# Optimization experiments

Hardware: AMD Instinct MI355X
Metric: run time of the kernel (lower is better)

The kernel has to match this reference:

```python
import jax, jax.numpy as jnp
import numpy as np

B, T, L, D, H = 8, 8192, 256, 512, 8
HD = D // H  # head_dim = 64


def setup_inputs() -> dict:
    key = jax.random.key(0)
    ks = jax.random.split(key, 6)
    s = 0.02
    return {
        "x": jax.random.normal(ks[0], (B, T, D), jnp.float32),
        "query": jax.random.normal(ks[1], (B, L, D), jnp.float32),
        "Wq": jax.random.normal(ks[2], (D, D), jnp.float32) * s,
        "bq": jnp.zeros((D,), jnp.float32),
        "Wkv": jax.random.normal(ks[3], (D, 2 * D), jnp.float32) * s,
        "bkv": jnp.zeros((2 * D,), jnp.float32),
        "Wproj": jax.random.normal(ks[4], (D, D), jnp.float32) * s,
        "bproj": jnp.zeros((D,), jnp.float32),
    }


def reference(x, query, Wq, bq, Wkv, bkv, Wproj, bproj):
    scale = HD ** (-0.5)
    # projections (weights stored [in, out]; equivalent to torch Linear with W.T)
    q = (query @ Wq + bq).reshape(B, L, H, HD).transpose(0, 2, 1, 3)   # [B,H,L,hd]
    kv = (x @ Wkv + bkv).reshape(B, T, 2, H, HD)
    k = kv[:, :, 0].transpose(0, 2, 1, 3)                              # [B,H,T,hd]
    v = kv[:, :, 1].transpose(0, 2, 1, 3)                              # [B,H,T,hd]
    # scaled dot-product attention, full L x T scores as in original
    attn = jnp.einsum("bhld,bhtd->bhlt", q * scale, k)                 # [B,H,L,T]
    attn = jax.nn.softmax(attn, axis=-1)
    out = jnp.einsum("bhlt,bhtd->bhld", attn, v)                       # [B,H,L,hd]
    out = out.transpose(0, 2, 1, 3).reshape(B, L, D)
    return out @ Wproj + bproj
```

## Files before the change

kernel.cpp:

```cpp
#include <hip/hip_runtime.h>
#include <hip/hip_bf16.h>
#include <cstdint>
#include <cstddef>

typedef __bf16 bf16_t;
typedef __bf16 bf16x8 __attribute__((ext_vector_type(8)));
typedef __bf16 bf16x4 __attribute__((ext_vector_type(4)));
typedef float  f32x4  __attribute__((ext_vector_type(4)));

#define DEVI __device__ __forceinline__

constexpr int B_ = 8, T_ = 8192, L_ = 256, D_ = 512, H_ = 8, HD_ = 64;
constexpr float SCALE_LOG2E = 0.125f * 1.44269504088896340736f;
constexpr int NSPLIT = 8;

DEVI float fast_exp2(float x) {
#if __has_builtin(__builtin_amdgcn_exp2f)
  return __builtin_amdgcn_exp2f(x);
#else
  return exp2f(x);
#endif
}

DEVI void async16(void* lds_base, const void* gptr, int lane) {
#if __has_builtin(__builtin_amdgcn_global_load_lds)
  __builtin_amdgcn_global_load_lds(
      (__attribute__((address_space(1))) void*)gptr,
      (__attribute__((address_space(3))) void*)lds_base, 16, 0, 0);
  (void)lane;
#else
  ((bf16x8*)lds_base)[lane] = *(const bf16x8*)gptr;
#endif
}

__global__ __launch_bounds__(256) void cvt_f32_to_bf16(
    const float* __restrict__ in, bf16_t* __restrict__ out, int n4) {
  int stride = gridDim.x * blockDim.x;
  for (int i = blockIdx.x * blockDim.x + threadIdx.x; i < n4; i += stride) {
    float4 v = ((const float4*)in)[i];
    bf16x4 o;
    o[0] = (bf16_t)v.x; o[1] = (bf16_t)v.y; o[2] = (bf16_t)v.z; o[3] = (bf16_t)v.w;
    ((bf16x4*)out)[i] = o;
  }
}

__global__ __launch_bounds__(256) void transpose_cvt(
    const float* __restrict__ W, bf16_t* __restrict__ WT, int K, int N, float scale) {
  __shared__ float tile[32][33];
  const int tx = threadIdx.x & 31, ty = threadIdx.x >> 5;
  const int n0 = blockIdx.x * 32, k0 = blockIdx.y * 32;
#pragma unroll
  for (int i = 0; i < 4; ++i)
    tile[ty + i * 8][tx] = W[(size_t)(k0 + ty + i * 8) * N + n0 + tx];
  __syncthreads();
#pragma unroll
  for (int i = 0; i < 4; ++i)
    WT[(size_t)(n0 + ty + i * 8) * K + k0 + tx] = (bf16_t)(tile[tx][ty + i * 8] * scale);
}

template <int MODE>
__global__ __launch_bounds__(256, 4) void gemm_bf16(
    const bf16_t* __restrict__ A, const bf16_t* __restrict__ BT,
    const float* __restrict__ bias, float bscale,
    bf16_t* __restrict__ out0,
    float* __restrict__ outf) {
  constexpr int K = 512;
  __shared__ __align__(16) union SM {
    bf16_t stage[2][128 * 64];
    bf16_t cs[128 * 136];
  } sm;

  const int tid = threadIdx.x;
  const int w = tid >> 6, lane = tid & 63;
  const int m0 = blockIdx.x * 128, n0 = blockIdx.y * 128;
  const int wm = w & 1, wn = w >> 1;

  f32x4 acc[4][4] = {};

  const int sw = ((lane & 7) ^ ((lane >> 3) & 7)) * 8;
  const bf16_t* aG = A + (size_t)(m0 + w * 32 + (lane >> 3)) * K + sw;
  const bf16_t* bG = BT + (size_t)(n0 + w * 32 + (lane >> 3)) * K + sw;
  bf16_t* aL = &sm.stage[0][(w * 32) * 64];
  bf16_t* bL = &sm.stage[1][(w * 32) * 64];

  for (int k0 = 0; k0 < K; k0 += 64) {
#pragma unroll
    for (int i = 0; i < 4; ++i) {
      async16(aL + i * (8 * 64), aG + k0 + (size_t)(i * 8) * K, lane);
      async16(bL + i * (8 * 64), bG + k0 + (size_t)(i * 8) * K, lane);
    }
    __syncthreads();
#pragma unroll
    for (int kk = 0; kk < 2; ++kk) {
      bf16x8 af[4], bfr[4];
      const int cc = ((kk * 4 + (lane >> 4)) ^ (lane & 7)) * 8;
#pragma unroll
      for (int mt = 0; mt < 4; ++mt)
        af[mt] = *(const bf16x8*)&sm.stage[0][(wm * 64 + mt * 16 + (lane & 15)) * 64 + cc];
#pragma unroll
      for (int nt = 0; nt < 4; ++nt)
        bfr[nt] = *(const bf16x8*)&sm.stage[1][(wn * 64 + nt * 16 + (lane & 15)) * 64 + cc];
#pragma unroll
      for (int mt = 0; mt < 4; ++mt)
#pragma unroll
        for (int nt = 0; nt < 4; ++nt)
          acc[mt][nt] = __builtin_amdgcn_mfma_f32_16x16x32_bf16(af[mt], bfr[nt], acc[mt][nt], 0, 0, 0);
    }
    __syncthreads();
  }

  if (MODE == 2) {
#pragma unroll
    for (int nt = 0; nt < 4; ++nt) {
      const int col = n0 + wn * 64 + nt * 16 + (lane & 15);
      const float bv = bias[col];
#pragma unroll
      for (int mt = 0; mt < 4; ++mt)
#pragma unroll
        for (int r = 0; r < 4; ++r) {
          const int row = m0 + wm * 64 + mt * 16 + (lane >> 4) * 4 + r;
          outf[(size_t)row * D_ + col] = acc[mt][nt][r] + bv;
        }
    }
    return;
  }

#pragma unroll
  for (int nt = 0; nt < 4; ++nt) {
    const int col = wn * 64 + nt * 16 + (lane & 15);
    const float bv = bias[n0 + col] * bscale;
#pragma unroll
    for (int mt = 0; mt < 4; ++mt)
#pragma unroll
      for (int r = 0; r < 4; ++r) {
        const int row = wm * 64 + mt * 16 + (lane >> 4) * 4 + r;
        sm.cs[row * 136 + col] = (bf16_t)(acc[mt][nt][r] + bv);
      }
  }
  __syncthreads();

#pragma unroll
  for (int i = 0; i < 8; ++i) {
    const int c = tid + i * 256;
    const int row = c >> 4, col = (c & 15) * 8;
    const int gr = m0 + row;
    const int b = gr >> 8, l = gr & 255;
    const int h = (n0 + col) >> 6, hd = (n0 + col) & 63;
    *(float4*)&out0[((size_t)(b * 8 + h) * L_ + l) * 64 + hd] =
        *(const float4*)&sm.cs[row * 136 + col];
  }
}

__global__ __launch_bounds__(512, 2) void gemm_kv(
    const bf16_t* __restrict__ A, const bf16_t* __restrict__ BT,
    const float* __restrict__ bias,
    bf16_t* __restrict__ kh, bf16_t* __restrict__ vTh) {
  constexpr int K = 512;
  __shared__ __align__(16) union SM {
    bf16_t stage[2][2][256 * 64];
    bf16_t cs[128 * 264];
  } sm;

  const int tid = threadIdx.x;
  const int w = tid >> 6, lane = tid & 63;
  const int wm = w & 1, wn = w >> 1;

  const int b = blockIdx.x;
  const int xcd = b & 7, idx = b >> 3;
  const int m0 = ((xcd << 5) | (idx >> 2)) * 256;
  const int n0 = (idx & 3) * 256;

  f32x4 acc[8][4] = {};

  const int sw = ((lane & 7) ^ ((lane >> 3) & 7)) * 8;
  const int rl = w * 8 + (lane >> 3);

  {
    bf16_t* As = sm.stage[0][0];
    bf16_t* Bs = sm.stage[0][1];
#pragma unroll
    for (int i = 0; i < 4; ++i)
      async16(As + (i * 64 + w * 8) * 64, A + (size_t)(m0 + i * 64 + rl) * K + sw, lane);
#pragma unroll
    for (int i = 0; i < 4; ++i)
      async16(Bs + (i * 64 + w * 8) * 64, BT + (size_t)(n0 + i * 64 + rl) * K + sw, lane);
  }

  for (int t = 0; t < 8; ++t) {
    __syncthreads();
    if (t < 7) {
      bf16_t* As = sm.stage[(t + 1) & 1][0];
      bf16_t* Bs = sm.stage[(t + 1) & 1][1];
      const int k0 = (t + 1) * 64;
#pragma unroll
      for (int i = 0; i < 4; ++i)
        async16(As + (i * 64 + w * 8) * 64, A + (size_t)(m0 + i * 64 + rl) * K + k0 + sw, lane);
#pragma unroll
      for (int i = 0; i < 4; ++i)
        async16(Bs + (i * 64 + w * 8) * 64, BT + (size_t)(n0 + i * 64 + rl) * K + k0 + sw, lane);
    }
    const bf16_t* As = sm.stage[t & 1][0];
    const bf16_t* Bs = sm.stage[t & 1][1];
#pragma unroll
    for (int kk = 0; kk < 2; ++kk) {
      const int cc = ((kk * 4 + (lane >> 4)) ^ (lane & 7)) * 8;
      bf16x8 bfr[4];
#pragma unroll
      for (int nt = 0; nt < 4; ++nt)
        bfr[nt] = *(const bf16x8*)&Bs[(wn * 64 + nt * 16 + (lane & 15)) * 64 + cc];
#pragma unroll
      for (int mh = 0; mh < 2; ++mh) {
        bf16x8 af[4];
#pragma unroll
        for (int mt = 0; mt < 4; ++mt)
          af[mt] = *(const bf16x8*)&As[(wm * 128 + (mh * 4 + mt) * 16 + (lane & 15)) * 64 + cc];
#pragma unroll
        for (int mt = 0; mt < 4; ++mt)
#pragma unroll
          for (int nt = 0; nt < 4; ++nt)
            acc[mh * 4 + mt][nt] = __builtin_amdgcn_mfma_f32_16x16x32_bf16(
                af[mt], bfr[nt], acc[mh * 4 + mt][nt], 0, 0, 0);
      }
    }
  }
  __syncthreads();

  float bv[4];
#pragma unroll
  for (int nt = 0; nt < 4; ++nt)
    bv[nt] = bias[n0 + wn * 64 + nt * 16 + (lane & 15)];

  if (n0 < 512) {
#pragma unroll
    for (int mh = 0; mh < 2; ++mh) {
      if (wm == mh) {
#pragma unroll
        for (int a = 0; a < 8; ++a)
#pragma unroll
          for (int nt = 0; nt < 4; ++nt)
#pragma unroll
            for (int r = 0; r < 4; ++r) {
              const int rowL = a * 16 + (lane >> 4) * 4 + r;
              const int col = wn * 64 + nt * 16 + (lane & 15);
              sm.cs[rowL * 264 + col] = (bf16_t)(acc[a][nt][r] + bv[nt]);
            }
      }
      __syncthreads();
#pragma unroll
      for (int i = 0; i < 8; ++i) {
        const int c = tid + i * 512;
        const int row = c >> 5, col = (c & 31) * 8;
        const int gr = m0 + mh * 128 + row;
        const int bb = gr >> 13, tt = gr & 8191;
        const int h = (n0 + col) >> 6, hd = (n0 + col) & 63;
        *(float4*)&kh[((size_t)(bb * 8 + h) * T_ + tt) * 64 + hd] =
            *(const float4*)&sm.cs[row * 264 + col];
      }
      __syncthreads();
    }
  } else {
    const int bb = m0 >> 13, t0 = m0 & 8191;
#pragma unroll
    for (int nh = 0; nh < 2; ++nh) {
      if ((wn >> 1) == nh) {
#pragma unroll
        for (int a = 0; a < 8; ++a)
#pragma unroll
          for (int nt = 0; nt < 4; ++nt)
#pragma unroll
            for (int r = 0; r < 4; ++r) {
              const int row = wm * 128 + a * 16 + (lane >> 4) * 4 + r;
              const int colL = (wn & 1) * 64 + nt * 16 + (lane & 15);
              sm.cs[colL * 264 + row] = (bf16_t)(acc[a][nt][r] + bv[nt]);
            }
      }
      __syncthreads();
#pragma unroll
      for (int i = 0; i < 8; ++i) {
        const int c = tid + i * 512;
        const int colL = c >> 5, tb = (c & 31) * 8;
        const int ch = (n0 - 512) + nh * 128 + colL;
        const int h = ch >> 6, hd = ch & 63;
        *(float4*)&vTh[((size_t)(bb * 8 + h) * 64 + hd) * T_ + t0 + tb] =
            *(const float4*)&sm.cs[colL * 264 + tb];
      }
      __syncthreads();
    }
  }
}

__global__ __launch_bounds__(256, 4) void attn_fwd(
    const bf16_t* __restrict__ qg, const bf16_t* __restrict__ kg,
    const bf16_t* __restrict__ vg, float* __restrict__ Opart,
    float* __restrict__ lbuf) {
  __shared__ __align__(16) bf16_t KPs[10240];
  __shared__ __align__(16) bf16_t Vs[4 * 64 * 32];
  bf16_t* Ks = KPs;
  bf16_t* Ps = KPs;
  bf16_t* Qs = KPs;

  const int n = blockIdx.x;
  const int split = n & 7, qt = (n >> 3) & 3, bh = n >> 5;
  const int tid = threadIdx.x;
  const int w = tid >> 6, lane = tid & 63;

  {
    const bf16_t* src = qg + ((size_t)bh * L_ + qt * 64) * 64;
    const int row = w * 16 + (lane >> 2);
#pragma unroll
    for (int hh = 0; hh < 2; ++hh)
      async16(&Qs[hh * 2048 + (w * 16) * 32],
              src + (size_t)row * 64 + hh * 32 + (lane & 3) * 8, lane);
  }
  __syncthreads();

  bf16x8 aq[2];
#pragma unroll
  for (int hh = 0; hh < 2; ++hh)
    aq[hh] = *(const bf16x8*)&Qs[hh * 2048 + (w * 16 + (lane & 15)) * 32 + (lane >> 4) * 8];
  __syncthreads();

  bf16x8 ones;
#pragma unroll
  for (int j = 0; j < 8; ++j) ones[j] = (bf16_t)1.0f;

  f32x4 O[4] = {};
  f32x4 lacc = {0.f, 0.f, 0.f, 0.f};

  const int kt0 = split * (T_ / 128 / NSPLIT);
  for (int kt = kt0; kt < kt0 + T_ / 128 / NSPLIT; ++kt) {
#pragma unroll
    for (int hh = 0; hh < 2; ++hh)
#pragma unroll
      for (int i = 0; i < 2; ++i) {
        const int trow = kt * 128 + w * 32 + i * 16 + (lane >> 2);
        async16(&Ks[hh * 4096 + (w * 32 + i * 16) * 32],
                kg + ((size_t)bh * T_ + trow) * 64 + hh * 32 + (lane & 3) * 8, lane);
      }
#pragma unroll
    for (int kc = 0; kc < 4; ++kc) {
      const int hd = w * 16 + (lane >> 2);
      async16(&Vs[kc * 2048 + (w * 16) * 32],
              vg + ((size_t)bh * 64 + hd) * T_ + kt * 128 + kc * 32 + (lane & 3) * 8, lane);
    }
    __syncthreads();

    f32x4 S[8];
#pragma unroll
    for (int nt = 0; nt < 8; ++nt) {
      bf16x8 b0 = *(const bf16x8*)&Ks[0 * 4096 + (nt * 16 + (lane & 15)) * 32 + (lane >> 4) * 8];
      bf16x8 b1 = *(const bf16x8*)&Ks[1 * 4096 + (nt * 16 + (lane & 15)) * 32 + (lane >> 4) * 8];
      f32x4 s = {0.f, 0.f, 0.f, 0.f};
      s = __builtin_amdgcn_mfma_f32_16x16x32_bf16(aq[0], b0, s, 0, 0, 0);
      s = __builtin_amdgcn_mfma_f32_16x16x32_bf16(aq[1], b1, s, 0, 0, 0);
#pragma unroll
      for (int r = 0; r < 4; ++r) s[r] = fast_exp2(s[r]);
      S[nt] = s;
    }

    __syncthreads();

#pragma unroll
    for (int nt = 0; nt < 8; ++nt)
#pragma unroll
      for (int r = 0; r < 4; ++r) {
        const int rp = w * 16 + (lane >> 4) * 4 + r;
        Ps[(nt >> 1) * 2560 + rp * 40 + (nt & 1) * 16 + (lane & 15)] = (bf16_t)S[nt][r];
      }

    __syncthreads();

#pragma unroll
    for (int kc = 0; kc < 4; ++kc) {
      bf16x8 ap = *(const bf16x8*)&Ps[kc * 2560 + (w * 16 + (lane & 15)) * 40 + (lane >> 4) * 8];
      lacc = __builtin_amdgcn_mfma_f32_16x16x32_bf16(ap, ones, lacc, 0, 0, 0);
#pragma unroll
      for (int n2 = 0; n2 < 4; ++n2) {
        bf16x8 bv = *(const bf16x8*)&Vs[kc * 2048 + (n2 * 16 + (lane & 15)) * 32 + (lane >> 4) * 8];
        O[n2] = __builtin_amdgcn_mfma_f32_16x16x32_bf16(ap, bv, O[n2], 0, 0, 0);
      }
    }
    __syncthreads();
  }

  const int part = ((bh * 4 + qt) * NSPLIT + split);
  float* op = Opart + (size_t)part * 64 * 64;
#pragma unroll
  for (int n2 = 0; n2 < 4; ++n2) {
#pragma unroll
    for (int r = 0; r < 4; ++r) {
      const int row = w * 16 + (lane >> 4) * 4 + r;
      op[(size_t)row * 64 + n2 * 16 + (lane & 15)] = O[n2][r];
    }
  }
  if ((lane & 15) == 0) {
    float* lb = lbuf + (size_t)part * 64;
#pragma unroll
    for (int r = 0; r < 4; ++r)
      lb[w * 16 + (lane >> 4) * 4 + r] = lacc[r];
  }
}

__global__ __launch_bounds__(256) void attn_combine(
    const float* __restrict__ Opart, const float* __restrict__ lbuf,
    bf16_t* __restrict__ og) {
  const int blk = blockIdx.x;
  const int bh = blk >> 2, qt = blk & 3;
  const int tid = threadIdx.x;
  const int row = tid >> 2, c0 = (tid & 3) * 16;
  float L = 0.f;
#pragma unroll
  for (int s = 0; s < NSPLIT; ++s) L += lbuf[((size_t)blk * NSPLIT + s) * 64 + row];
  const float inv = 1.f / L;
  f32x4 acc[4] = {};
  const float* ob = Opart + (size_t)blk * NSPLIT * 4096 + row * 64 + c0;
#pragma unroll
  for (int s = 0; s < NSPLIT; ++s)
#pragma unroll
    for (int j = 0; j < 4; ++j) {
      f32x4 v = *(const f32x4*)&ob[s * 4096 + j * 4];
      acc[j] += v;
    }
  const int b = bh >> 3, h = bh & 7;
  bf16_t* dst = og + ((size_t)(b * L_ + qt * 64 + row)) * D_ + h * 64 + c0;
#pragma unroll
  for (int j = 0; j < 4; ++j) {
    bf16x4 o;
#pragma unroll
    for (int e = 0; e < 4; ++e) o[e] = (bf16_t)(acc[j][e] * inv);
    *(bf16x4*)&dst[j * 4] = o;
  }
}

extern "C" void kernel_launch(void* const* d_in, const int* in_sizes, int n_in,
                              void* d_out, int out_size, void* d_ws, size_t ws_size,
                              hipStream_t stream) {
  const float* x     = (const float*)d_in[0];
  const float* query = (const float*)d_in[1];
  const float* Wq    = (const float*)d_in[2];
  const float* bq    = (const float*)d_in[3];
  const float* Wkv   = (const float*)d_in[4];
  const float* bkv   = (const float*)d_in[5];
  const float* Wproj = (const float*)d_in[6];
  const float* bproj = (const float*)d_in[7];
  float* out = (float*)d_out;

  char* ws = (char*)d_ws;
  bf16_t* xb   = (bf16_t*)(ws + 0);
  float*  Opart = (float*)(ws + 0);
  float*  lbuf  = (float*)(ws + 34603008);
  bf16_t* wkvT = (bf16_t*)(ws + 67108864);
  bf16_t* wqT  = (bf16_t*)(ws + 68157440);
  bf16_t* qin  = (bf16_t*)(ws + 68681728);
  bf16_t* qh   = (bf16_t*)(ws + 70778880);
  bf16_t* kh   = (bf16_t*)(ws + 72876032);
  bf16_t* vTh  = (bf16_t*)(ws + 139984896);
  bf16_t* attnb = (bf16_t*)(ws + 207093760);
  bf16_t* wprojT = (bf16_t*)(ws + 209190912);

  cvt_f32_to_bf16<<<4096, 256, 0, stream>>>(x, xb, (B_ * T_ * D_) / 4);
  cvt_f32_to_bf16<<<1024, 256, 0, stream>>>(query, qin, (B_ * L_ * D_) / 4);
  transpose_cvt<<<dim3(16, 16), 256, 0, stream>>>(Wq, wqT, 512, 512, SCALE_LOG2E);
  transpose_cvt<<<dim3(32, 16), 256, 0, stream>>>(Wkv, wkvT, 512, 1024, 1.0f);
  transpose_cvt<<<dim3(16, 16), 256, 0, stream>>>(Wproj, wprojT, 512, 512, 1.0f);
  gemm_bf16<0><<<dim3(16, 4), 256, 0, stream>>>(qin, wqT, bq, SCALE_LOG2E, qh, nullptr);
  gemm_kv<<<dim3(1024), 512, 0, stream>>>(xb, wkvT, bkv, kh, vTh);
  attn_fwd<<<dim3(64 * 4 * NSPLIT), 256, 0, stream>>>(qh, kh, vTh, Opart, lbuf);
  attn_combine<<<dim3(256), 256, 0, stream>>>(Opart, lbuf, attnb);
  gemm_bf16<2><<<dim3(16, 4), 256, 0, stream>>>(attnb, wprojT, bproj, 1.0f, nullptr, out);
}
```

Baseline: 395.4 us.

## Software-pipeline KV projection GEMM with register double-buffered fragments and setprio

Restructures the main KV projection GEMM main loop so that A and B fragments are loaded into register sets (ra0/ra1, rb0/rb1) in quadrants. The LDS reads for the next quadrant are interleaved with MFMA blocks, separated by explicit s_barrier calls, and the next k-tile's global-to-LDS copy is issued early. It also raises wave priority around MFMA clusters with s_setprio. The goal is to hide LDS latency and global load latency behind matrix math. The cost is higher register pressure and many extra barriers. The async16 helper signature is also simplified by dropping the unused lane argument.

```diff
diff --git a/kernel.cpp b/kernel.cpp
--- a/kernel.cpp
+++ b/kernel.cpp
@@ -22,14 +22,13 @@
 #endif
 }
 
-DEVI void async16(void* lds_base, const void* gptr, int lane) {
+DEVI void async16(void* lds_base, const void* gptr) {
 #if __has_builtin(__builtin_amdgcn_global_load_lds)
   __builtin_amdgcn_global_load_lds(
       (__attribute__((address_space(1))) void*)gptr,
       (__attribute__((address_space(3))) void*)lds_base, 16, 0, 0);
-  (void)lane;
 #else
-  ((bf16x8*)lds_base)[lane] = *(const bf16x8*)gptr;
+  ((bf16x8*)lds_base)[threadIdx.x & 63] = *(const bf16x8*)gptr;
 #endif
 }
 
@@ -86,8 +85,8 @@
   for (int k0 = 0; k0 < K; k0 += 64) {
 #pragma unroll
     for (int i = 0; i < 4; ++i) {
-      async16(aL + i * (8 * 64), aG + k0 + (size_t)(i * 8) * K, lane);
-      async16(bL + i * (8 * 64), bG + k0 + (size_t)(i * 8) * K, lane);
+      async16(aL + i * (8 * 64), aG + k0 + (size_t)(i * 8) * K);
+      async16(bL + i * (8 * 64), bG + k0 + (size_t)(i * 8) * K);
     }
     __syncthreads();
 #pragma unroll
@@ -174,54 +173,82 @@
 
   const int sw = ((lane & 7) ^ ((lane >> 3) & 7)) * 8;
   const int rl = w * 8 + (lane >> 3);
-
-  {
-    bf16_t* As = sm.stage[0][0];
-    bf16_t* Bs = sm.stage[0][1];
+  const bf16_t* aG = A + (size_t)(m0 + rl) * K + sw;
+  const bf16_t* bG = BT + (size_t)(n0 + rl) * K + sw;
+  bf16_t* SS = &sm.stage[0][0][0];
+
+  const int la = lane & 15;
+  const int cc0 = ((lane >> 4) ^ (lane & 7)) * 8;
+  const int cc1 = ((4 + (lane >> 4)) ^ (lane & 7)) * 8;
+
+  bf16x8 ra0[8], ra1[8], rb0[4], rb1[4];
+
+  auto stage_pair = [&](int bufo, int k0) {
+    bf16_t* dA = SS + bufo + (w * 8) * 64;
+    bf16_t* dB = SS + bufo + 16384 + (w * 8) * 64;
 #pragma unroll
     for (int i = 0; i < 4; ++i)
-      async16(As + (i * 64 + w * 8) * 64, A + (size_t)(m0 + i * 64 + rl) * K + sw, lane);
+      async16(dA + i * 4096, aG + k0 + (size_t)(i * 64) * K);
 #pragma unroll
     for (int i = 0; i < 4; ++i)
-      async16(Bs + (i * 64 + w * 8) * 64, BT + (size_t)(n0 + i * 64 + rl) * K + sw, lane);
-  }
-
+      async16(dB + i * 4096, bG + k0 + (size_t)(i * 64) * K);
+  };
+  auto ld_a = [&](bf16x8* r, const bf16_t* base, int mq) {
+#pragma unroll
+    for (int mt = 0; mt < 4; ++mt) {
+      r[mt * 2]     = *(const bf16x8*)&base[(mq * 64 + mt * 16 + la) * 64 + cc0];
+      r[mt * 2 + 1] = *(const bf16x8*)&base[(mq * 64 + mt * 16 + la) * 64 + cc1];
+    }
+  };
+  auto ld_b = [&](bf16x8* r, const bf16_t* base, int nq) {
+#pragma unroll
+    for (int ntl = 0; ntl < 2; ++ntl) {
+      r[ntl * 2]     = *(const bf16x8*)&base[((nq * 2 + ntl) * 16 + la) * 64 + cc0];
+      r[ntl * 2 + 1] = *(const bf16x8*)&base[((nq * 2 + ntl) * 16 + la) * 64 + cc1];
+    }
+  };
+  auto mm8 = [&](const bf16x8* ra, const bf16x8* rb, int mq, int nq) {
+    __builtin_amdgcn_s_setprio(1);
+#pragma unroll
+    for (int mt = 0; mt < 4; ++mt)
+#pragma unroll
+      for (int ntl = 0; ntl < 2; ++ntl) {
+        f32x4& c = acc[mq * 4 + mt][nq * 2 + ntl];
+        c = __builtin_amdgcn_mfma_f32_16x16x32_bf16(ra[mt * 2],     rb[ntl * 2],     c, 0, 0, 0);
+        c = __builtin_amdgcn_mfma_f32_16x16x32_bf16(ra[mt * 2 + 1], rb[ntl * 2 + 1], c, 0, 0, 0);
+      }
+    __builtin_amdgcn_s_setprio(0);
+  };
+
+  stage_pair(0, 0);
+  asm volatile("s_waitcnt vmcnt(0)" ::: "memory");
+  __builtin_amdgcn_s_barrier();
+  ld_a(ra0, SS + wm * 8192, 0);
+
+#pragma unroll
   for (int t = 0; t < 8; ++t) {
-    __syncthreads();
+    const int Xo = (t & 1) * 32768, Yo = ((t + 1) & 1) * 32768;
+    const bf16_t* Ax = SS + Xo + wm * 8192;
+    const bf16_t* Bx = SS + Xo + 16384 + wn * 4096;
+    ld_b(rb0, Bx, 0);
+    ld_b(rb1, Bx, 1);
+    if (t < 7) stage_pair(Yo, (t + 1) * 64);
+    __builtin_amdgcn_s_barrier();
+    mm8(ra0, rb0, 0, 0);
+    __builtin_amdgcn_s_barrier();
+    ld_a(ra1, Ax, 1);
+    __builtin_amdgcn_s_barrier();
+    mm8(ra0, rb1, 0, 1);
+    __builtin_amdgcn_s_barrier();
+    mm8(ra1, rb1, 1, 1);
+    __builtin_amdgcn_s_barrier();
     if (t < 7) {
-      bf16_t* As = sm.stage[(t + 1) & 1][0];
-      bf16_t* Bs = sm.stage[(t + 1) & 1][1];
-      const int k0 = (t + 1) * 64;
-#pragma unroll
-      for (int i = 0; i < 4; ++i)
-        async16(As + (i * 64 + w * 8) * 64, A + (size_t)(m0 + i * 64 + rl) * K + k0 + sw, lane);
-#pragma unroll
-      for (int i = 0; i < 4; ++i)
-        async16(Bs + (i * 64 + w * 8) * 64, BT + (size_t)(n0 + i * 64 + rl) * K + k0 + sw, lane);
-    }
-    const bf16_t* As = sm.stage[t & 1][0];
-    const bf16_t* Bs = sm.stage[t & 1][1];
-#pragma unroll
-    for (int kk = 0; kk < 2; ++kk) {
-      const int cc = ((kk * 4 + (lane >> 4)) ^ (lane & 7)) * 8;
-      bf16x8 bfr[4];
-#pragma unroll
-      for (int nt = 0; nt < 4; ++nt)
-        bfr[nt] = *(const bf16x8*)&Bs[(wn * 64 + nt * 16 + (lane & 15)) * 64 + cc];
-#pragma unroll
-      for (int mh = 0; mh < 2; ++mh) {
-        bf16x8 af[4];
-#pragma unroll
-        for (int mt = 0; mt < 4; ++mt)
-          af[mt] = *(const bf16x8*)&As[(wm * 128 + (mh * 4 + mt) * 16 + (lane & 15)) * 64 + cc];
-#pragma unroll
-        for (int mt = 0; mt < 4; ++mt)
-#pragma unroll
-          for (int nt = 0; nt < 4; ++nt)
-            acc[mh * 4 + mt][nt] = __builtin_amdgcn_mfma_f32_16x16x32_bf16(
-                af[mt], bfr[nt], acc[mh * 4 + mt][nt], 0, 0, 0);
-      }
-    }
+      asm volatile("s_waitcnt vmcnt(0)" ::: "memory");
+      __builtin_amdgcn_s_barrier();
+      ld_a(ra0, SS + Yo + wm * 8192, 0);
+    }
+    mm8(ra1, rb0, 1, 0);
+    __builtin_amdgcn_s_barrier();
   }
   __syncthreads();
 
@@ -310,7 +337,7 @@
 #pragma unroll
     for (int hh = 0; hh < 2; ++hh)
       async16(&Qs[hh * 2048 + (w * 16) * 32],
-              src + (size_t)row * 64 + hh * 32 + (lane & 3) * 8, lane);
+              src + (size_t)row * 64 + hh * 32 + (lane & 3) * 8);
   }
   __syncthreads();
 
@@ -335,13 +362,13 @@
       for (int i = 0; i < 2; ++i) {
         const int trow = kt * 128 + w * 32 + i * 16 + (lane >> 2);
         async16(&Ks[hh * 4096 + (w * 32 + i * 16) * 32],
-                kg + ((size_t)bh * T_ + trow) * 64 + hh * 32 + (lane & 3) * 8, lane);
+                kg + ((size_t)bh * T_ + trow) * 64 + hh * 32 + (lane & 3) * 8);
       }
 #pragma unroll
     for (int kc = 0; kc < 4; ++kc) {
       const int hd = w * 16 + (lane >> 2);
       async16(&Vs[kc * 2048 + (w * 16) * 32],
-              vg + ((size_t)bh * 64 + hd) * T_ + kt * 128 + kc * 32 + (lane & 3) * 8, lane);
+              vg + ((size_t)bh * 64 + hd) * T_ + kt * 128 + kc * 32 + (lane & 3) * 8);
     }
     __syncthreads();
 
```

Result: slower. 404.7 us (+2.4%).
